# Performance work log

Measured on AMD Instinct MI355X. Metric: run time of the kernel, lower is better.

## Reference

```python
import jax, jax.numpy as jnp
import numpy as np

EMBED_DIM = 768
NUM_HEADS = 12
D_K = EMBED_DIM // NUM_HEADS


def setup_inputs() -> dict:
    key = jax.random.key(0)
    ks = jax.random.split(key, 9)
    b, s, d = 4, 2048, EMBED_DIM
    scale = 1.0 / np.sqrt(d)
    x = jax.random.normal(ks[0], (b, s, d), dtype=jnp.float32)
    return {
        "x": x,
        "w_q": jax.random.normal(ks[1], (d, d), dtype=jnp.float32) * scale,
        "b_q": jnp.zeros((d,), dtype=jnp.float32),
        "w_k": jax.random.normal(ks[2], (d, d), dtype=jnp.float32) * scale,
        "b_k": jnp.zeros((d,), dtype=jnp.float32),
        "w_v": jax.random.normal(ks[3], (d, d), dtype=jnp.float32) * scale,
        "b_v": jnp.zeros((d,), dtype=jnp.float32),
        "w_o": jax.random.normal(ks[4], (d, d), dtype=jnp.float32) * scale,
        "b_o": jnp.zeros((d,), dtype=jnp.float32),
    }


def reference(x, w_q, b_q, w_k, b_k, w_v, b_v, w_o, b_o):
    b, s, d = x.shape
    h, dk = NUM_HEADS, D_K
    # projections (torch Linear: x @ W^T + b)
    q = (x @ w_q.T + b_q).reshape(b, s, h, dk).transpose(0, 2, 1, 3)
    k = (x @ w_k.T + b_k).reshape(b, s, h, dk).transpose(0, 2, 1, 3)
    v = (x @ w_v.T + b_v).reshape(b, s, h, dk).transpose(0, 2, 1, 3)
    # causal attention: full [b,h,s,s] scores as in the original
    scores = jnp.einsum("bhqd,bhkd->bhqk", q, k) / jnp.sqrt(jnp.float32(dk))
    causal = jnp.tril(jnp.ones((s, s), dtype=bool))
    scores = jnp.where(causal[None, None], scores, -jnp.inf)
    attn = jax.nn.softmax(scores, axis=-1)
    out = jnp.einsum("bhqk,bhkd->bhqd", attn, v)
    out = out.transpose(0, 2, 1, 3).reshape(b, s, h * dk)
    return out @ w_o.T + b_o
```

## Files before the change

kernel.cpp:

```cpp
#include <hip/hip_runtime.h>
#include <hip/hip_bf16.h>
#include <stdint.h>

typedef short bf16x8 __attribute__((ext_vector_type(8)));
typedef float f32x4 __attribute__((ext_vector_type(4)));
typedef unsigned short u16;


__device__ __forceinline__ u16 f2bf_bits(float f) {
    __hip_bfloat16 h = __float2bfloat16(f);
    return __builtin_bit_cast(u16, h);
}

__device__ __forceinline__ uint32_t pack2bf(float a, float b) {
    uint32_t ua = __builtin_bit_cast(uint32_t, a) + 0x8000u;
    uint32_t ub = __builtin_bit_cast(uint32_t, b) + 0x8000u;
    return __builtin_amdgcn_perm(ub, ua, 0x07060302u);
}

__device__ __forceinline__ void gld_lds16(const void* g, void* l) {
    __builtin_amdgcn_global_load_lds(
        (const __attribute__((address_space(1))) void*)g,
        (__attribute__((address_space(3))) void*)l, 16, 0, 0);
}

#define CEXP 0.18033688011112042f


__global__ __launch_bounds__(256) void cast_all_kernel(
    const float* __restrict__ x, const float* __restrict__ w0,
    const float* __restrict__ w1, const float* __restrict__ w2,
    const float* __restrict__ w3, u16* __restrict__ xb,
    u16* __restrict__ o0, u16* __restrict__ o1,
    u16* __restrict__ o2, u16* __restrict__ o3,
    const float* __restrict__ bq, const float* __restrict__ bk,
    const float* __restrict__ bv, float* __restrict__ biasf) {
    int gid = blockIdx.x * 256 + threadIdx.x;
    const float* s;
    u16* d;
    int off;
    if (gid < 1572864) {
        s = x; d = xb; off = gid;
    } else {
        int g2 = gid - 1572864;
        int which = g2 / 147456;
        off = g2 - which * 147456;
        s = which == 0 ? w0 : which == 1 ? w1 : which == 2 ? w2 : w3;
        d = which == 0 ? o0 : which == 1 ? o1 : which == 2 ? o2 : o3;
    }
    float4 v = ((const float4*)s)[off];
    ushort4 u;
    u.x = f2bf_bits(v.x); u.y = f2bf_bits(v.y);
    u.z = f2bf_bits(v.z); u.w = f2bf_bits(v.w);
    ((ushort4*)d)[off] = u;
    if (gid < 2304) {
        float bb = gid < 768 ? bq[gid] : gid < 1536 ? bk[gid - 768] : bv[gid - 1536];
        biasf[gid] = bb;
    }
}


template <int RT, int MODE>
__global__ __launch_bounds__(256) void gemm_xwt(
    const u16* __restrict__ X, const u16* __restrict__ W,
    const float* __restrict__ bias, float* __restrict__ Cf,
    u16* __restrict__ Cb, u16* __restrict__ Vt, int K, int NC, int NTIL) {
    constexpr int JR = RT / 32;
    __shared__ u16 lsX[RT * 64];
    __shared__ u16 lsW[128 * 64];
    const int tid = threadIdx.x;
    const int w = tid >> 6, lane = tid & 63;
    const int quad = lane >> 4, l15 = lane & 15;
    const int cpx = gridDim.x >> 3;
    const int sb = (blockIdx.x & 7) * cpx + (blockIdx.x >> 3);
    const int mt = sb / NTIL, nt = sb - mt * NTIL;
    const int m0 = mt * RT, n0 = nt * 128;
    const int wr = (w >> 1) * (RT / 2), wc = (w & 1) * 64;
    const int rr = lane >> 3, c8 = lane & 7;

    f32x4 acc[JR][4];
    for (int j = 0; j < JR; ++j)
        for (int i = 0; i < 4; ++i) acc[j][i] = (f32x4){0.f, 0.f, 0.f, 0.f};

    const int KT = K / 64;
    for (int kt = 0; kt < KT; ++kt) {
        const int k0 = kt * 64;
        __syncthreads();
        for (int cb = w; cb < RT / 8; cb += 4) {
            int row = cb * 8 + rr;
            int cg = c8 ^ ((rr ^ cb) & 7);
            gld_lds16(X + (size_t)(m0 + row) * K + k0 + cg * 8, &lsX[cb * 512]);
        }
        for (int cb = w; cb < 16; cb += 4) {
            int row = cb * 8 + rr;
            int cg = c8 ^ ((rr ^ cb) & 7);
            gld_lds16(W + (size_t)(n0 + row) * K + k0 + cg * 8, &lsW[cb * 512]);
        }
        __syncthreads();

        for (int kk = 0; kk < 2; ++kk) {
            bf16x8 xf[JR], wf[4];
            for (int j = 0; j < JR; ++j) {
                int row = wr + j * 16 + l15;
                int slot = (kk * 4 + quad) ^ ((row ^ (row >> 3)) & 7);
                xf[j] = *(const bf16x8*)&lsX[row * 64 + slot * 8];
            }
            for (int i = 0; i < 4; ++i) {
                int row = wc + i * 16 + l15;
                int slot = (kk * 4 + quad) ^ ((row ^ (row >> 3)) & 7);
                wf[i] = *(const bf16x8*)&lsW[row * 64 + slot * 8];
            }
            for (int j = 0; j < JR; ++j)
                for (int i = 0; i < 4; ++i)
                    acc[j][i] = __builtin_amdgcn_mfma_f32_16x16x32_bf16(
                        wf[i], xf[j], acc[j][i], 0, 0, 0);
        }
    }

    const bool vtile = (MODE == 2) && (n0 >= 1536);
    for (int i = 0; i < 4; ++i) {
        int c0 = n0 + wc + i * 16 + quad * 4;
        float4 bv4 = *(const float4*)&bias[c0];
        for (int j = 0; j < JR; ++j) {
            int row = m0 + wr + j * 16 + l15;
            float v0 = acc[j][i][0] + bv4.x;
            float v1 = acc[j][i][1] + bv4.y;
            float v2 = acc[j][i][2] + bv4.z;
            float v3 = acc[j][i][3] + bv4.w;
            if (MODE == 1) {
                float4 o4 = {v0, v1, v2, v3};
                *(float4*)&Cf[(size_t)row * NC + c0] = o4;
            } else if (vtile) {
                int d = c0 - 1536;
                int bq_ = row >> 11;
                int s = row & 2047;
                int h = d >> 6, dd = d & 63;
                size_t base = ((size_t)(bq_ * 12 + h) * 64 + dd) * 2048 + s;
                Vt[base]          = f2bf_bits(v0);
                Vt[base + 2048]   = f2bf_bits(v1);
                Vt[base + 4096]   = f2bf_bits(v2);
                Vt[base + 6144]   = f2bf_bits(v3);
            } else {
                float sc = (MODE == 2 && c0 < 768) ? CEXP : 1.0f;
                uint2 pk = {pack2bf(v0 * sc, v1 * sc), pack2bf(v2 * sc, v3 * sc)};
                *(uint2*)&Cb[(size_t)row * NC + c0] = pk;
            }
        }
    }
}


__global__ __launch_bounds__(256, 3) void attn_kernel(
    const u16* __restrict__ QKV, const u16* __restrict__ Vt, u16* __restrict__ O) {
    __shared__ u16 lsQ[128 * 64];
    __shared__ u16 lsK0[64 * 64];
    __shared__ u16 lsV0[64 * 64];
    __shared__ u16 lsP[4][32 * 72];

    int bx = blockIdx.x;
    int bh = bx % 48;
    int j  = bx / 48;
    const int ta = j;
    const int tb = 31 - j;
    int bb = bh / 12, h = bh % 12;
    int tid = threadIdx.x, w = tid >> 6, lane = tid & 63;
    int quad = lane >> 4, l15 = lane & 15;
    int rr = lane >> 3, c8 = lane & 7;

    u16* K1 = lsQ;
    u16* V1 = lsQ + 4096;

    const size_t kgbase = (size_t)(bb * 2048) * 2304 + 768 + (size_t)h * 64;
    const size_t vgbase = (size_t)(bh * 64) * 2048;

    auto stage = [&](int kt, u16* lsK, u16* lsV) {
        for (int cb = w; cb < 8; cb += 4) {
            int row = cb * 8 + rr;
            int cg = c8 ^ ((rr ^ cb) & 7);
            gld_lds16(QKV + kgbase + (size_t)(kt * 64 + row) * 2304 + cg * 8,
                      &lsK[cb * 512]);
            gld_lds16(Vt + vgbase + (size_t)row * 2048 + kt * 64 + cg * 8,
                      &lsV[cb * 512]);
        }
    };

    for (int cb = w; cb < 16; cb += 4) {
        int row = cb * 8 + rr;
        int qrow = (row < 64) ? ta * 64 + row : tb * 64 + (row - 64);
        int cg = c8 ^ ((rr ^ cb) & 7);
        gld_lds16(QKV + (size_t)(bb * 2048 + qrow) * 2304 + h * 64 + cg * 8,
                  &lsQ[cb * 512]);
    }
    stage(0, lsK0, lsV0);
    __syncthreads();

    bf16x8 q0[2], q1[2];
    for (int g = 0; g < 2; ++g) {
        int rowq = g * 64 + w * 16 + l15;
        int swq = (rowq ^ (rowq >> 3)) & 7;
        q0[g] = *(const bf16x8*)&lsQ[rowq * 64 + ((0 + quad) ^ swq) * 8];
        q1[g] = *(const bf16x8*)&lsQ[rowq * 64 + ((4 + quad) ^ swq) * 8];
    }
    __syncthreads();

    f32x4 oacc0[4], oacc1[4];
    for (int dt = 0; dt < 4; ++dt) {
        oacc0[dt] = (f32x4){0.f, 0.f, 0.f, 0.f};
        oacc1[dt] = (f32x4){0.f, 0.f, 0.f, 0.f};
    }
    float li0 = 0.f, li1 = 0.f;
    u16* Pw = lsP[w];
    const int qrel = w * 16 + l15;

    auto compute = [&](int kt, const u16* lsK, const u16* lsV) {
        const bool do0 = (kt <= ta);

        f32x4 S0[4], S1[4];
        __builtin_amdgcn_s_setprio(1);
        for (int ct = 0; ct < 4; ++ct) {
            int rowk = ct * 16 + l15;
            int swk = (rowk ^ (rowk >> 3)) & 7;
            bf16x8 k0 = *(const bf16x8*)&lsK[rowk * 64 + ((0 + quad) ^ swk) * 8];
            bf16x8 k1 = *(const bf16x8*)&lsK[rowk * 64 + ((4 + quad) ^ swk) * 8];
            f32x4 z = (f32x4){0.f, 0.f, 0.f, 0.f};
            S1[ct] = __builtin_amdgcn_mfma_f32_16x16x32_bf16(k0, q0[1], z, 0, 0, 0);
            S1[ct] = __builtin_amdgcn_mfma_f32_16x16x32_bf16(k1, q1[1], S1[ct], 0, 0, 0);
            if (do0) {
                S0[ct] = __builtin_amdgcn_mfma_f32_16x16x32_bf16(k0, q0[0], z, 0, 0, 0);
                S0[ct] = __builtin_amdgcn_mfma_f32_16x16x32_bf16(k1, q1[0], S0[ct], 0, 0, 0);
            }
        }
        __builtin_amdgcn_s_setprio(0);

        if (kt == ta) {
            for (int ct = 0; ct < 4; ++ct) {
                int kbase = ct * 16 + quad * 4;
                for (int r = 0; r < 4; ++r)
                    if (kbase + r > qrel) S0[ct][r] = -1e30f;
            }
        }
        if (kt == tb) {
            for (int ct = 0; ct < 4; ++ct) {
                int kbase = ct * 16 + quad * 4;
                for (int r = 0; r < 4; ++r)
                    if (kbase + r > qrel) S1[ct][r] = -1e30f;
            }
        }

        if (do0) {
            u16* Pr = &Pw[(size_t)l15 * 72];
            for (int ct = 0; ct < 4; ++ct) {
                float p0 = __builtin_amdgcn_exp2f(S0[ct][0]);
                float p1 = __builtin_amdgcn_exp2f(S0[ct][1]);
                float p2 = __builtin_amdgcn_exp2f(S0[ct][2]);
                float p3 = __builtin_amdgcn_exp2f(S0[ct][3]);
                li0 += (p0 + p1) + (p2 + p3);
                uint2 pk = {pack2bf(p0, p1), pack2bf(p2, p3)};
                *(uint2*)&Pr[ct * 16 + quad * 4] = pk;
            }
        }
        {
            u16* Pr = &Pw[(size_t)(16 + l15) * 72];
            for (int ct = 0; ct < 4; ++ct) {
                float p0 = __builtin_amdgcn_exp2f(S1[ct][0]);
                float p1 = __builtin_amdgcn_exp2f(S1[ct][1]);
                float p2 = __builtin_amdgcn_exp2f(S1[ct][2]);
                float p3 = __builtin_amdgcn_exp2f(S1[ct][3]);
                li1 += (p0 + p1) + (p2 + p3);
                uint2 pk = {pack2bf(p0, p1), pack2bf(p2, p3)};
                *(uint2*)&Pr[ct * 16 + quad * 4] = pk;
            }
        }

        __builtin_amdgcn_s_setprio(1);
        for (int ks = 0; ks < 2; ++ks) {
            bf16x8 bp1 = *(const bf16x8*)&Pw[(size_t)(16 + l15) * 72 + ks * 32 + quad * 8];
            bf16x8 bp0;
            if (do0) bp0 = *(const bf16x8*)&Pw[(size_t)l15 * 72 + ks * 32 + quad * 8];
            for (int dt = 0; dt < 4; ++dt) {
                int rowv = dt * 16 + l15;
                int swv = (rowv ^ (rowv >> 3)) & 7;
                bf16x8 av = *(const bf16x8*)&lsV[rowv * 64 + ((ks * 4 + quad) ^ swv) * 8];
                oacc1[dt] = __builtin_amdgcn_mfma_f32_16x16x32_bf16(av, bp1, oacc1[dt], 0, 0, 0);
                if (do0)
                    oacc0[dt] = __builtin_amdgcn_mfma_f32_16x16x32_bf16(av, bp0, oacc0[dt], 0, 0, 0);
            }
        }
        __builtin_amdgcn_s_setprio(0);
    };

    for (int kt = 0; kt + 1 <= tb; kt += 2) {
        stage(kt + 1, K1, V1);
        compute(kt, lsK0, lsV0);
        __syncthreads();
        if (kt + 2 <= tb) stage(kt + 2, lsK0, lsV0);
        compute(kt + 1, K1, V1);
        __syncthreads();
    }
    if ((tb & 1) == 0) compute(tb, lsK0, lsV0);

    li0 += __shfl_xor(li0, 16, 64);
    li0 += __shfl_xor(li0, 32, 64);
    li1 += __shfl_xor(li1, 16, 64);
    li1 += __shfl_xor(li1, 32, 64);
    float inv0 = 1.0f / li0, inv1 = 1.0f / li1;

    for (int g = 0; g < 2; ++g) {
        float inv = g ? inv1 : inv0;
        f32x4* oa = g ? oacc1 : oacc0;
        int row = (g ? tb : ta) * 64 + w * 16 + l15;
        for (int dt = 0; dt < 4; ++dt) {
            uint2 pk = {pack2bf(oa[dt][0] * inv, oa[dt][1] * inv),
                        pack2bf(oa[dt][2] * inv, oa[dt][3] * inv)};
            *(uint2*)&O[(size_t)(bb * 2048 + row) * 768 + h * 64 + dt * 16 + quad * 4] = pk;
        }
    }
}


extern "C" void kernel_launch(void* const* d_in, const int* in_sizes, int n_in,
                              void* d_out, int out_size, void* d_ws, size_t ws_size,
                              hipStream_t stream) {
    const float* x  = (const float*)d_in[0];
    const float* wq = (const float*)d_in[1];
    const float* bq = (const float*)d_in[2];
    const float* wk = (const float*)d_in[3];
    const float* bk = (const float*)d_in[4];
    const float* wv = (const float*)d_in[5];
    const float* bv = (const float*)d_in[6];
    const float* wo = (const float*)d_in[7];
    const float* bo = (const float*)d_in[8];
    float* out = (float*)d_out;

    char* ws = (char*)d_ws;
    u16*   xb    = (u16*)(ws + 0);
    u16*   Wf    = (u16*)(ws + 12582912);
    u16*   wob   = (u16*)(ws + 16121856);
    float* biasf = (float*)(ws + 17301504);
    u16*   QKVb  = (u16*)(ws + 17310720);
    u16*   Vtw   = (u16*)(ws + 55059456);
    u16*   Ow    = (u16*)(ws + 67642368);

    cast_all_kernel<<<8448, 256, 0, stream>>>(x, wq, wk, wv, wo,
                                              xb, Wf, Wf + 589824, Wf + 1179648, wob,
                                              bq, bk, bv, biasf);

    gemm_xwt<128, 2><<<1152, 256, 0, stream>>>(xb, Wf, biasf, nullptr, QKVb,
                                               Vtw, 768, 2304, 18);
    attn_kernel<<<768, 256, 0, stream>>>(QKVb, Vtw, Ow);
    gemm_xwt<64, 1><<<768, 256, 0, stream>>>(Ow, wob, bo, out, nullptr,
                                             nullptr, 768, 768, 6);
}
```

Baseline: 204.5 us.

## Fuse fp32-to-bf16 casts into GEMM tile loads and drop the cast kernel

Removes the separate cast kernel that turned x and all weights into bf16 in workspace. The GEMMs now read fp32 x and weights directly, pack them to bf16 in registers and store them into swizzled LDS, and read biases straight from the input arrays. This saves one launch and a full round trip of x and the weights through memory. In exchange, the async global-to-LDS loads become synchronous register loads of twice the bytes, and each weight tile is re-converted by every block that uses it.

```diff
diff --git a/kernel.cpp b/kernel.cpp
--- a/kernel.cpp
+++ b/kernel.cpp
@@ -27,44 +27,15 @@
 #define CEXP 0.18033688011112042f
 
 
-__global__ __launch_bounds__(256) void cast_all_kernel(
-    const float* __restrict__ x, const float* __restrict__ w0,
-    const float* __restrict__ w1, const float* __restrict__ w2,
-    const float* __restrict__ w3, u16* __restrict__ xb,
-    u16* __restrict__ o0, u16* __restrict__ o1,
-    u16* __restrict__ o2, u16* __restrict__ o3,
-    const float* __restrict__ bq, const float* __restrict__ bk,
-    const float* __restrict__ bv, float* __restrict__ biasf) {
-    int gid = blockIdx.x * 256 + threadIdx.x;
-    const float* s;
-    u16* d;
-    int off;
-    if (gid < 1572864) {
-        s = x; d = xb; off = gid;
-    } else {
-        int g2 = gid - 1572864;
-        int which = g2 / 147456;
-        off = g2 - which * 147456;
-        s = which == 0 ? w0 : which == 1 ? w1 : which == 2 ? w2 : w3;
-        d = which == 0 ? o0 : which == 1 ? o1 : which == 2 ? o2 : o3;
-    }
-    float4 v = ((const float4*)s)[off];
-    ushort4 u;
-    u.x = f2bf_bits(v.x); u.y = f2bf_bits(v.y);
-    u.z = f2bf_bits(v.z); u.w = f2bf_bits(v.w);
-    ((ushort4*)d)[off] = u;
-    if (gid < 2304) {
-        float bb = gid < 768 ? bq[gid] : gid < 1536 ? bk[gid - 768] : bv[gid - 1536];
-        biasf[gid] = bb;
-    }
-}
-
-
 template <int RT, int MODE>
 __global__ __launch_bounds__(256) void gemm_xwt(
-    const u16* __restrict__ X, const u16* __restrict__ W,
-    const float* __restrict__ bias, float* __restrict__ Cf,
-    u16* __restrict__ Cb, u16* __restrict__ Vt, int K, int NC, int NTIL) {
+    const void* __restrict__ Xv,
+    const float* __restrict__ w0, const float* __restrict__ w1,
+    const float* __restrict__ w2,
+    const float* __restrict__ b0, const float* __restrict__ b1,
+    const float* __restrict__ b2,
+    float* __restrict__ Cf, u16* __restrict__ Cb, u16* __restrict__ Vt,
+    int K, int NC, int NTIL) {
     constexpr int JR = RT / 32;
     __shared__ u16 lsX[RT * 64];
     __shared__ u16 lsW[128 * 64];
@@ -78,6 +49,16 @@
     const int wr = (w >> 1) * (RT / 2), wc = (w & 1) * 64;
     const int rr = lane >> 3, c8 = lane & 7;
 
+    const float* Ws;
+    int nw0;
+    if (MODE == 2) {
+        Ws  = n0 < 768 ? w0 : n0 < 1536 ? w1 : w2;
+        nw0 = n0 < 768 ? n0 : n0 < 1536 ? n0 - 768 : n0 - 1536;
+    } else {
+        Ws = w0;
+        nw0 = n0;
+    }
+
     f32x4 acc[JR][4];
     for (int j = 0; j < JR; ++j)
         for (int i = 0; i < 4; ++i) acc[j][i] = (f32x4){0.f, 0.f, 0.f, 0.f};
@@ -88,13 +69,29 @@
         __syncthreads();
         for (int cb = w; cb < RT / 8; cb += 4) {
             int row = cb * 8 + rr;
-            int cg = c8 ^ ((rr ^ cb) & 7);
-            gld_lds16(X + (size_t)(m0 + row) * K + k0 + cg * 8, &lsX[cb * 512]);
+            if (MODE == 2) {
+                const float* src = (const float*)Xv + (size_t)(m0 + row) * K + k0 + c8 * 8;
+                float4 a = *(const float4*)src;
+                float4 b = *(const float4*)(src + 4);
+                uint4 pk = {pack2bf(a.x, a.y), pack2bf(a.z, a.w),
+                            pack2bf(b.x, b.y), pack2bf(b.z, b.w)};
+                int sl = c8 ^ ((rr ^ cb) & 7);
+                *(uint4*)&lsX[cb * 512 + rr * 64 + sl * 8] = pk;
+            } else {
+                int cg = c8 ^ ((rr ^ cb) & 7);
+                gld_lds16((const u16*)Xv + (size_t)(m0 + row) * K + k0 + cg * 8,
+                          &lsX[cb * 512]);
+            }
         }
         for (int cb = w; cb < 16; cb += 4) {
             int row = cb * 8 + rr;
-            int cg = c8 ^ ((rr ^ cb) & 7);
-            gld_lds16(W + (size_t)(n0 + row) * K + k0 + cg * 8, &lsW[cb * 512]);
+            const float* src = Ws + (size_t)(nw0 + row) * K + k0 + c8 * 8;
+            float4 a = *(const float4*)src;
+            float4 b = *(const float4*)(src + 4);
+            uint4 pk = {pack2bf(a.x, a.y), pack2bf(a.z, a.w),
+                        pack2bf(b.x, b.y), pack2bf(b.z, b.w)};
+            int sl = c8 ^ ((rr ^ cb) & 7);
+            *(uint4*)&lsW[cb * 512 + rr * 64 + sl * 8] = pk;
         }
         __syncthreads();
 
@@ -120,7 +117,10 @@
     const bool vtile = (MODE == 2) && (n0 >= 1536);
     for (int i = 0; i < 4; ++i) {
         int c0 = n0 + wc + i * 16 + quad * 4;
-        float4 bv4 = *(const float4*)&bias[c0];
+        const float* bp = (MODE == 2)
+            ? (c0 < 768 ? b0 + c0 : c0 < 1536 ? b1 + (c0 - 768) : b2 + (c0 - 1536))
+            : b0 + c0;
+        float4 bv4 = *(const float4*)bp;
         for (int j = 0; j < JR; ++j) {
             int row = m0 + wr + j * 16 + l15;
             float v0 = acc[j][i][0] + bv4.x;
@@ -333,21 +333,14 @@
     float* out = (float*)d_out;
 
     char* ws = (char*)d_ws;
-    u16*   xb    = (u16*)(ws + 0);
-    u16*   Wf    = (u16*)(ws + 12582912);
-    u16*   wob   = (u16*)(ws + 16121856);
-    float* biasf = (float*)(ws + 17301504);
     u16*   QKVb  = (u16*)(ws + 17310720);
     u16*   Vtw   = (u16*)(ws + 55059456);
     u16*   Ow    = (u16*)(ws + 67642368);
 
-    cast_all_kernel<<<8448, 256, 0, stream>>>(x, wq, wk, wv, wo,
-                                              xb, Wf, Wf + 589824, Wf + 1179648, wob,
-                                              bq, bk, bv, biasf);
-
-    gemm_xwt<128, 2><<<1152, 256, 0, stream>>>(xb, Wf, biasf, nullptr, QKVb,
-                                               Vtw, 768, 2304, 18);
+    gemm_xwt<128, 2><<<1152, 256, 0, stream>>>(x, wq, wk, wv, bq, bk, bv,
+                                               nullptr, QKVb, Vtw, 768, 2304, 18);
     attn_kernel<<<768, 256, 0, stream>>>(QKVb, Vtw, Ow);
-    gemm_xwt<64, 1><<<768, 256, 0, stream>>>(Ow, wob, bo, out, nullptr,
-                                             nullptr, 768, 768, 6);
-}
+    gemm_xwt<64, 1><<<768, 256, 0, stream>>>(Ow, wo, nullptr, nullptr,
+                                             bo, nullptr, nullptr,
+                                             out, nullptr, nullptr, 768, 768, 6);
+}
```

Result: slower. 260.6 us (+27.4%).
